# Kernel tuning notes

Hardware: AMD Instinct MI355X
Metric: run time of the kernel (lower is better)

The kernel has to match this reference:

```python
import jax, jax.numpy as jnp
import numpy as np

B, N, C = 2, 4096, 512
H = 8
K = 512  # num pivotal tokens


def setup_inputs() -> dict:
    key = jax.random.key(0)
    k1, k2, k3 = jax.random.split(key, 3)
    x = jax.random.normal(k1, (B, N, C), dtype=jnp.float32)
    w_qkv = jax.random.normal(k2, (C, 3 * C), dtype=jnp.float32) * (C ** -0.5)
    w_proj = jax.random.normal(k3, (C, C), dtype=jnp.float32) * (C ** -0.5)
    b_proj = jnp.zeros((C,), dtype=jnp.float32)
    return {"x": x, "w_qkv": w_qkv, "w_proj": w_proj, "b_proj": b_proj,
            "num_heads": H, "num_pivots": K}


def reference(x, w_qkv, w_proj, b_proj, num_heads, num_pivots):
    b, n, c = x.shape
    h = num_heads
    d = c // h
    scale = d ** -0.5
    # qkv projection -> q, k, v each [b, h, n, d]
    qkv = (x @ w_qkv).reshape(b, n, 3, h, d)
    q, k, v = jnp.moveaxis(qkv, 2, 0)          # each [b, n, h, d]
    q = jnp.swapaxes(q, 1, 2)                  # [b, h, n, d]
    k = jnp.swapaxes(k, 1, 2)
    v = jnp.swapaxes(v, 1, 2)
    # raw attention scores, materialized (the custom-kernel hotspot)
    attn = jax.nn.softmax(jnp.einsum('bhqd,bhkd->bhqk', q, k) * scale, axis=-1)
    # standard attention output + projection
    out = jnp.einsum('bhqk,bhkd->bhqd', attn, v)       # [b, h, n, d]
    out = jnp.swapaxes(out, 1, 2).reshape(b, n, c)     # [b, n, c]
    out = out @ w_proj + b_proj
    # pivotal-token importance: attention mass each token receives,
    # averaged over heads and queries -> [b, n]
    importance = attn.mean(axis=1).mean(axis=1)
    _, idx = jax.lax.top_k(importance, num_pivots)     # [b, K]
    # gather pivotal tokens -> reduced sequence [b, K, c]
    pivots = jnp.take_along_axis(out, idx[:, :, None], axis=1)
    return pivots
```

## Files before the change

kernel.cpp:

```cpp
#include <hip/hip_runtime.h>
#include <hip/hip_bf16.h>

#define BB 2
#define NN 4096
#define CC 512
#define HH 8
#define DD 64
#define KPIV 512
#define SCALE 0.125f
#define C2INV 4.8828125e-4f
#define C2    2048.0f

typedef unsigned short ushort_t;
typedef __attribute__((ext_vector_type(8))) short short8;
typedef __attribute__((ext_vector_type(8))) _Float16 half8;
typedef __attribute__((ext_vector_type(16))) float float16;

__device__ __forceinline__ float bf2f(ushort_t h) {
    union { unsigned u; float f; } x; x.u = ((unsigned)h) << 16; return x.f;
}
__device__ __forceinline__ ushort_t f2bf(float f) {
    __hip_bfloat16 h = __float2bfloat16(f);
    ushort_t u;
    __builtin_memcpy(&u, &h, sizeof(u));
    return u;
}
__device__ __forceinline__ void split2h(float x, _Float16& hi, _Float16& lo) {
    hi = (_Float16)x;
    lo = (_Float16)((x - (float)hi) * C2);
}

__global__ __launch_bounds__(256) void qkv_gemm_k(
    const float* __restrict__ x, const float* __restrict__ w,
    float* __restrict__ q, _Float16* __restrict__ khg, _Float16* __restrict__ klg,
    ushort_t* __restrict__ v)
{
    __shared__ __attribute__((aligned(16))) float xs[16][132];
    __shared__ __attribute__((aligned(16))) float ws[16][132];
    const int t = threadIdx.x;
    const int row0 = blockIdx.x * 128;
    const int col0 = blockIdx.y * 128;
    const int tr = t & 15, tc = t >> 4;
    const int ts = col0 >> 9;
    float acc[8][8] = {};
    for (int k0 = 0; k0 < CC; k0 += 16) {
        __syncthreads();
        {
            const int r = t >> 1, off = (t & 1) * 8;
            const float* xp = x + (size_t)(row0 + r) * CC + k0 + off;
            float4 v0 = *(const float4*)xp;
            float4 v1 = *(const float4*)(xp + 4);
            xs[off + 0][r] = v0.x; xs[off + 1][r] = v0.y;
            xs[off + 2][r] = v0.z; xs[off + 3][r] = v0.w;
            xs[off + 4][r] = v1.x; xs[off + 5][r] = v1.y;
            xs[off + 6][r] = v1.z; xs[off + 7][r] = v1.w;
        }
        {
            const int kk = t >> 4, c8 = (t & 15) * 8;
            const float* wp2 = w + (size_t)(k0 + kk) * (3 * CC) + col0 + c8;
            *(float4*)&ws[kk][c8]     = *(const float4*)wp2;
            *(float4*)&ws[kk][c8 + 4] = *(const float4*)(wp2 + 4);
        }
        __syncthreads();
        #pragma unroll
        for (int kk = 0; kk < 16; ++kk) {
            float a[8], b[8];
            *(float4*)&a[0] = *(const float4*)&xs[kk][tr * 8];
            *(float4*)&a[4] = *(const float4*)&xs[kk][tr * 8 + 4];
            *(float4*)&b[0] = *(const float4*)&ws[kk][tc * 8];
            *(float4*)&b[4] = *(const float4*)&ws[kk][tc * 8 + 4];
            #pragma unroll
            for (int i = 0; i < 8; ++i)
                #pragma unroll
                for (int j = 0; j < 8; ++j)
                    acc[i][j] = fmaf(a[i], b[j], acc[i][j]);
        }
    }
    const int gc0 = col0 + tc * 8;
    const int hh = (gc0 >> 6) & 7;
    const int dd0 = gc0 & 63;
    #pragma unroll
    for (int i = 0; i < 8; ++i) {
        const int grow = row0 + tr * 8 + i;
        const int b = grow >> 12, n = grow & (NN - 1);
        const size_t base = (((size_t)b * HH + hh) * NN + n) * DD + dd0;
        if (ts == 0) {
            float4 v0, v1;
            v0.x = acc[i][0]; v0.y = acc[i][1]; v0.z = acc[i][2]; v0.w = acc[i][3];
            v1.x = acc[i][4]; v1.y = acc[i][5]; v1.z = acc[i][6]; v1.w = acc[i][7];
            *(float4*)(q + base) = v0;
            *(float4*)(q + base + 4) = v1;
        } else if (ts == 1) {
            half8 h8, l8;
            #pragma unroll
            for (int j = 0; j < 8; ++j) {
                _Float16 a2, b2; split2h(acc[i][j], a2, b2);
                h8[j] = a2; l8[j] = b2;
            }
            *(half8*)(khg + base) = h8;
            *(half8*)(klg + base) = l8;
        } else {
            #pragma unroll
            for (int j = 0; j < 8; ++j)
                v[(((size_t)b * HH + hh) * DD + dd0 + j) * NN + n] = f2bf(acc[i][j]);
        }
    }
}


__device__ __forceinline__ void load_q_frags_h(
    const float* __restrict__ q, size_t row, int g, half8* qh, half8* ql)
{
    const float* qp = q + row * DD + g * 8;
    #pragma unroll
    for (int kd = 0; kd < 4; ++kd) {
        float4 f0 = *(const float4*)(qp + kd * 16);
        float4 f1 = *(const float4*)(qp + kd * 16 + 4);
        float xv[8] = {f0.x, f0.y, f0.z, f0.w, f1.x, f1.y, f1.z, f1.w};
        #pragma unroll
        for (int j = 0; j < 8; ++j) {
            _Float16 a2, b2; split2h(xv[j] * SCALE, a2, b2);
            qh[kd][j] = a2; ql[kd][j] = b2;
        }
    }
}

__device__ __forceinline__ void stage_k128(
    const _Float16* __restrict__ khg, const _Float16* __restrict__ klg,
    int bh, int n0, int t, half8* khs, half8* kls)
{
    const _Float16* kb = khg + ((size_t)bh * NN + n0) * DD;
    const _Float16* lb = klg + ((size_t)bh * NN + n0) * DD;
    #pragma unroll
    for (int j = 0; j < 4; ++j) {
        const int s = t + j * 256;
        const int seg = s >> 7, tok = s & 127;
        const size_t off = (size_t)tok * DD + seg * 8;
        uint4 uh = *(const uint4*)(kb + off);
        uint4 ul = *(const uint4*)(lb + off);
        *(uint4*)&khs[seg * 128 + tok] = uh;
        *(uint4*)&kls[seg * 128 + tok] = ul;
    }
}

#define S_MFMA_STEP(t0)                                                       \
    float16 a0, a12;                                                          \
    _Pragma("unroll")                                                         \
    for (int i = 0; i < 16; ++i) { a0[i] = 0.f; a12[i] = 0.f; }               \
    _Pragma("unroll")                                                         \
    for (int kd = 0; kd < 4; ++kd) {                                          \
        half8 bhi = khs[(kd * 2 + g) * 128 + (t0) + ln];                      \
        half8 blo = kls[(kd * 2 + g) * 128 + (t0) + ln];                      \
        a0  = __builtin_amdgcn_mfma_f32_32x32x16_f16(qh[kd], bhi, a0, 0,0,0); \
        a12 = __builtin_amdgcn_mfma_f32_32x32x16_f16(ql[kd], bhi, a12,0,0,0); \
        a12 = __builtin_amdgcn_mfma_f32_32x32x16_f16(qh[kd], blo, a12,0,0,0); \
    }

__global__ __launch_bounds__(256) void pass_a_k(
    const float* __restrict__ q, const _Float16* __restrict__ khg,
    const _Float16* __restrict__ klg, float* __restrict__ l)
{
    __shared__ half8 khs[8 * 128];
    __shared__ half8 kls[8 * 128];
    const int t = threadIdx.x;
    const int lane = t & 63, wv = t >> 6;
    const int g = lane >> 5, ln = lane & 31;
    const int bh = blockIdx.x >> 5;
    const int qt = blockIdx.x & 31;
    half8 qh[4], ql[4];
    load_q_frags_h(q, (size_t)bh * NN + qt * 128 + wv * 32 + ln, g, qh, ql);
    float rowacc[16];
    #pragma unroll
    for (int r = 0; r < 16; ++r) rowacc[r] = 0.f;
    for (int n0 = 0; n0 < NN; n0 += 128) {
        __syncthreads();
        stage_k128(khg, klg, bh, n0, t, khs, kls);
        __syncthreads();
        #pragma unroll
        for (int ii = 0; ii < 4; ++ii) {
            S_MFMA_STEP(ii * 32)
            #pragma unroll
            for (int r = 0; r < 16; ++r)
                rowacc[r] += __expf(fmaf(a12[r], C2INV, a0[r]));
        }
    }
    #pragma unroll
    for (int r = 0; r < 16; ++r) {
        float vs = rowacc[r];
        vs += __shfl_xor(vs, 1);
        vs += __shfl_xor(vs, 2);
        vs += __shfl_xor(vs, 4);
        vs += __shfl_xor(vs, 8);
        vs += __shfl_xor(vs, 16);
        rowacc[r] = vs;
    }
    if (ln == 0) {
        #pragma unroll
        for (int r = 0; r < 16; ++r) {
            const int row = (r & 3) + 8 * (r >> 2) + 4 * g;
            l[(size_t)bh * NN + qt * 128 + wv * 32 + row] = rowacc[r];
        }
    }
}

__global__ __launch_bounds__(256) void pass_b_k(
    const float* __restrict__ q, const _Float16* __restrict__ khg,
    const _Float16* __restrict__ klg, const float* __restrict__ l,
    float* __restrict__ colsum)
{
    __shared__ half8 khs[8 * 128];
    __shared__ half8 kls[8 * 128];
    __shared__ float colbuf[4][128];
    const int t = threadIdx.x;
    const int lane = t & 63, wv = t >> 6;
    const int g = lane >> 5, ln = lane & 31;
    const int bh = blockIdx.x >> 5;
    const int qt = blockIdx.x & 31;
    half8 qh[4], ql[4];
    load_q_frags_h(q, (size_t)bh * NN + qt * 128 + wv * 32 + ln, g, qh, ql);
    float rv[16];
    #pragma unroll
    for (int r = 0; r < 16; ++r) {
        const int row = (r & 3) + 8 * (r >> 2) + 4 * g;
        rv[r] = 1.0f / l[(size_t)bh * NN + qt * 128 + wv * 32 + row];
    }
    for (int n0 = 0; n0 < NN; n0 += 128) {
        __syncthreads();
        if (n0 > 0 && t < 128)
            colsum[(size_t)blockIdx.x * NN + (n0 - 128) + t] =
                (colbuf[0][t] + colbuf[1][t]) + (colbuf[2][t] + colbuf[3][t]);
        stage_k128(khg, klg, bh, n0, t, khs, kls);
        __syncthreads();
        #pragma unroll
        for (int ii = 0; ii < 4; ++ii) {
            S_MFMA_STEP(ii * 32)
            float cs = 0.f;
            #pragma unroll
            for (int r = 0; r < 16; ++r)
                cs = fmaf(__expf(fmaf(a12[r], C2INV, a0[r])), rv[r], cs);
            cs += __shfl_xor(cs, 32);
            if (g == 0) colbuf[wv][ii * 32 + ln] = cs;
        }
    }
    __syncthreads();
    if (t < 128)
        colsum[(size_t)blockIdx.x * NN + (NN - 128) + t] =
            (colbuf[0][t] + colbuf[1][t]) + (colbuf[2][t] + colbuf[3][t]);
}

__global__ __launch_bounds__(256) void imp_reduce_k(
    const float* __restrict__ colsum, double* __restrict__ imp)
{
    const int n = blockIdx.x * 256 + threadIdx.x;
    const int b = n >> 12, c = n & (NN - 1);
    const float* p = colsum + (size_t)b * 256 * NN + c;
    double s = 0.0;
    for (int i = 0; i < 256; ++i) s += (double)p[(size_t)i * NN];
    imp[n] = s * (1.0 / (double)(HH * NN));
}

__global__ __launch_bounds__(1024) void topk_k(
    const double* __restrict__ imp, int* __restrict__ idxout)
{
    __shared__ double sv[4096];
    __shared__ int si[4096];
    const int b = blockIdx.x, t = threadIdx.x;
    for (int i = t; i < 4096; i += 1024) { sv[i] = imp[b * 4096 + i]; si[i] = i; }
    __syncthreads();
    for (int kk = 2; kk <= 4096; kk <<= 1) {
        for (int j = kk >> 1; j > 0; j >>= 1) {
            #pragma unroll 1
            for (int r = 0; r < 2; ++r) {
                const int cm = t + r * 1024;
                const int i = ((cm & ~(j - 1)) << 1) | (cm & (j - 1));
                const int lo = i | j;
                const bool up = ((i & kk) == 0);
                const double va = sv[i], vb = sv[lo];
                const int ia = si[i], ib = si[lo];
                const bool after = (va < vb) || (va == vb && ia > ib);
                if (after == up) { sv[i] = vb; sv[lo] = va; si[i] = ib; si[lo] = ia; }
            }
            __syncthreads();
        }
    }
    if (t < KPIV) idxout[b * KPIV + t] = si[t];
}

__global__ __launch_bounds__(256) void pass_c_k(
    const float* __restrict__ q, const _Float16* __restrict__ khg,
    const _Float16* __restrict__ klg, const ushort_t* __restrict__ vt,
    const float* __restrict__ l, const int* __restrict__ idx,
    float* __restrict__ opiv)
{
    __shared__ short8 pfr[4][4][32];
    __shared__ __attribute__((aligned(16))) float osum[4][32][64];
    const int t = threadIdx.x;
    const int lane = t & 63, wv = t >> 6;
    const int g = lane >> 5, ln = lane & 31;
    const int bid = blockIdx.x;
    const int b = bid >> 8, h = (bid >> 5) & 7;
    const int chunk = (bid >> 1) & 15, th = bid & 1;
    const int bh = b * HH + h;
    const int r0 = chunk * 32;
    const int tokq = idx[b * KPIV + r0 + ln];
    half8 qh[4], ql[4];
    load_q_frags_h(q, (size_t)bh * NN + tokq, g, qh, ql);
    float rv[16];
    #pragma unroll
    for (int r = 0; r < 16; ++r) {
        const int row = (r & 3) + 8 * (r >> 2) + 4 * g;
        rv[r] = 1.0f / l[(size_t)bh * NN + idx[b * KPIV + r0 + row]];
    }
    float16 oacc0, oacc1;
    #pragma unroll
    for (int i = 0; i < 16; ++i) { oacc0[i] = 0.f; oacc1[i] = 0.f; }
    const int base_n = th * 2048 + wv * 512;
    for (int step = 0; step < 16; ++step) {
        const int n0 = base_n + step * 32;
        float16 a0, a12;
        #pragma unroll
        for (int i = 0; i < 16; ++i) { a0[i] = 0.f; a12[i] = 0.f; }
        const size_t koff = ((size_t)bh * NN + n0 + ln) * DD + g * 8;
        #pragma unroll
        for (int kd = 0; kd < 4; ++kd) {
            uint4 uh = *(const uint4*)(khg + koff + kd * 16);
            uint4 ul = *(const uint4*)(klg + koff + kd * 16);
            half8 bh8, bl8;
            __builtin_memcpy(&bh8, &uh, 16);
            __builtin_memcpy(&bl8, &ul, 16);
            a0  = __builtin_amdgcn_mfma_f32_32x32x16_f16(qh[kd], bh8, a0, 0,0,0);
            a12 = __builtin_amdgcn_mfma_f32_32x32x16_f16(ql[kd], bh8, a12,0,0,0);
            a12 = __builtin_amdgcn_mfma_f32_32x32x16_f16(qh[kd], bl8, a12,0,0,0);
        }
        __syncthreads();
        #pragma unroll
        for (int r = 0; r < 16; ++r) {
            const int row = (r & 3) + 8 * (r >> 2) + 4 * g;
            const float p = __expf(fmaf(a12[r], C2INV, a0[r])) * rv[r];
            *((ushort_t*)&pfr[wv][ln >> 3][row] + (ln & 7)) = f2bf(p);
        }
        __syncthreads();
        #pragma unroll
        for (int kh2 = 0; kh2 < 2; ++kh2) {
            short8 pa = pfr[wv][kh2 * 2 + g][ln];
            const ushort_t* vp0 = vt + ((size_t)bh * DD + ln) * NN + n0 + kh2 * 16 + g * 8;
            uint4 u0 = *(const uint4*)vp0;
            uint4 u1 = *(const uint4*)(vp0 + (size_t)32 * NN);
            short8 vb0, vb1;
            __builtin_memcpy(&vb0, &u0, 16);
            __builtin_memcpy(&vb1, &u1, 16);
            oacc0 = __builtin_amdgcn_mfma_f32_32x32x16_bf16(pa, vb0, oacc0, 0,0,0);
            oacc1 = __builtin_amdgcn_mfma_f32_32x32x16_bf16(pa, vb1, oacc1, 0,0,0);
        }
    }
    #pragma unroll
    for (int r = 0; r < 16; ++r) {
        const int row = (r & 3) + 8 * (r >> 2) + 4 * g;
        osum[wv][row][ln]      = oacc0[r];
        osum[wv][row][32 + ln] = oacc1[r];
    }
    __syncthreads();
    {
        const int qrow = t >> 3, d0 = (t & 7) * 8;
        float s[8] = {};
        #pragma unroll
        for (int w = 0; w < 4; ++w) {
            float4 a  = *(const float4*)&osum[w][qrow][d0];
            float4 b2 = *(const float4*)&osum[w][qrow][d0 + 4];
            s[0] += a.x;  s[1] += a.y;  s[2] += a.z;  s[3] += a.w;
            s[4] += b2.x; s[5] += b2.y; s[6] += b2.z; s[7] += b2.w;
        }
        float* op = opiv + ((size_t)(b * KPIV + r0 + qrow)) * CC + h * DD + d0;
        #pragma unroll
        for (int j = 0; j < 8; ++j) atomicAdd(op + j, s[j]);
    }
}

__global__ __launch_bounds__(256) void proj_k(
    const float* __restrict__ opiv, const float* __restrict__ wp,
    const float* __restrict__ bp, float* __restrict__ out)
{
    __shared__ __attribute__((aligned(16))) float os[8][CC];
    const int t = threadIdx.x;
    const int r0 = blockIdx.x * 8;
    for (int f = t; f < 1024; f += 256) {
        const int rr = f >> 7, i = (f & 127) * 4;
        *(float4*)&os[rr][i] = *(const float4*)(opiv + (size_t)(r0 + rr) * CC + i);
    }
    __syncthreads();
    const int c0 = t;
    float acc0[8] = {}, acc1[8] = {};
    for (int i = 0; i < CC; ++i) {
        const float w0 = wp[(size_t)i * CC + c0];
        const float w1 = wp[(size_t)i * CC + c0 + 256];
        #pragma unroll
        for (int rr = 0; rr < 8; ++rr) {
            const float ov = os[rr][i];
            acc0[rr] = fmaf(ov, w0, acc0[rr]);
            acc1[rr] = fmaf(ov, w1, acc1[rr]);
        }
    }
    const float b0 = bp[c0], b1 = bp[c0 + 256];
    #pragma unroll
    for (int rr = 0; rr < 8; ++rr) {
        out[((size_t)(r0 + rr)) * CC + c0]       = acc0[rr] + b0;
        out[((size_t)(r0 + rr)) * CC + c0 + 256] = acc1[rr] + b1;
    }
}

extern "C" void kernel_launch(void* const* d_in, const int* in_sizes, int n_in,
                              void* d_out, int out_size, void* d_ws, size_t ws_size,
                              hipStream_t stream)
{
    const float* x     = (const float*)d_in[0];
    const float* wqkv  = (const float*)d_in[1];
    const float* wproj = (const float*)d_in[2];
    const float* bproj = (const float*)d_in[3];

    float*     q      = (float*)d_ws;
    _Float16*  khg    = (_Float16*)(q + (size_t)BB * HH * NN * DD);
    _Float16*  klg    = khg + (size_t)BB * HH * NN * DD;
    ushort_t*  v      = (ushort_t*)(klg + (size_t)BB * HH * NN * DD);
    float*     l      = (float*)(v + (size_t)BB * HH * NN * DD);
    float*     colsum = l + (size_t)BB * HH * NN;
    double*    imp    = (double*)(colsum + (size_t)512 * NN);
    int*       idx    = (int*)(imp + BB * NN);
    float*     opiv   = (float*)(idx + BB * KPIV);
    float*     out    = (float*)d_out;

    const size_t need = (size_t)((char*)(opiv + (size_t)BB * KPIV * CC) - (char*)d_ws);
    if (ws_size < need) return;

    qkv_gemm_k<<<dim3(64, 12), 256, 0, stream>>>(x, wqkv, q, khg, klg, v);
    pass_a_k<<<512, 256, 0, stream>>>(q, khg, klg, l);
    pass_b_k<<<512, 256, 0, stream>>>(q, khg, klg, l, colsum);
    imp_reduce_k<<<32, 256, 0, stream>>>(colsum, imp);
    topk_k<<<2, 1024, 0, stream>>>(imp, idx);
    hipMemsetAsync(opiv, 0, (size_t)BB * KPIV * CC * sizeof(float), stream);
    pass_c_k<<<512, 256, 0, stream>>>(q, khg, klg, v, l, idx, opiv);
    proj_k<<<128, 256, 0, stream>>>(opiv, wproj, bproj, out);
}
```

Before: 689.4 us.

## Presplit Q into fp16 hi/lo in GEMM and read K directly from global

```diff
diff --git a/kernel.cpp b/kernel.cpp
--- a/kernel.cpp
+++ b/kernel.cpp
@@ -32,8 +32,9 @@
 
 __global__ __launch_bounds__(256) void qkv_gemm_k(
     const float* __restrict__ x, const float* __restrict__ w,
-    float* __restrict__ q, _Float16* __restrict__ khg, _Float16* __restrict__ klg,
-    ushort_t* __restrict__ v)
+    _Float16* __restrict__ qhg, _Float16* __restrict__ qlg,
+    _Float16* __restrict__ khg, _Float16* __restrict__ klg,
+    ushort_t* __restrict__ vt)
 {
     __shared__ __attribute__((aligned(16))) float xs[16][132];
     __shared__ __attribute__((aligned(16))) float ws[16][132];
@@ -85,11 +86,14 @@
         const int b = grow >> 12, n = grow & (NN - 1);
         const size_t base = (((size_t)b * HH + hh) * NN + n) * DD + dd0;
         if (ts == 0) {
-            float4 v0, v1;
-            v0.x = acc[i][0]; v0.y = acc[i][1]; v0.z = acc[i][2]; v0.w = acc[i][3];
-            v1.x = acc[i][4]; v1.y = acc[i][5]; v1.z = acc[i][6]; v1.w = acc[i][7];
-            *(float4*)(q + base) = v0;
-            *(float4*)(q + base + 4) = v1;
+            half8 h8, l8;
+            #pragma unroll
+            for (int j = 0; j < 8; ++j) {
+                _Float16 a2, b2; split2h(acc[i][j] * SCALE, a2, b2);
+                h8[j] = a2; l8[j] = b2;
+            }
+            *(half8*)(qhg + base) = h8;
+            *(half8*)(qlg + base) = l8;
         } else if (ts == 1) {
             half8 h8, l8;
             #pragma unroll
@@ -102,87 +106,58 @@
         } else {
             #pragma unroll
             for (int j = 0; j < 8; ++j)
-                v[(((size_t)b * HH + hh) * DD + dd0 + j) * NN + n] = f2bf(acc[i][j]);
-        }
-    }
-}
-
-
-__device__ __forceinline__ void load_q_frags_h(
-    const float* __restrict__ q, size_t row, int g, half8* qh, half8* ql)
-{
-    const float* qp = q + row * DD + g * 8;
+                vt[(((size_t)b * HH + hh) * DD + dd0 + j) * NN + n] = f2bf(acc[i][j]);
+        }
+    }
+}
+
+__device__ __forceinline__ void load_q_frags(
+    const _Float16* __restrict__ qhg, const _Float16* __restrict__ qlg,
+    size_t qrow, int g, half8* qh, half8* ql)
+{
+    const size_t off = qrow * DD + g * 8;
     #pragma unroll
     for (int kd = 0; kd < 4; ++kd) {
-        float4 f0 = *(const float4*)(qp + kd * 16);
-        float4 f1 = *(const float4*)(qp + kd * 16 + 4);
-        float xv[8] = {f0.x, f0.y, f0.z, f0.w, f1.x, f1.y, f1.z, f1.w};
-        #pragma unroll
-        for (int j = 0; j < 8; ++j) {
-            _Float16 a2, b2; split2h(xv[j] * SCALE, a2, b2);
-            qh[kd][j] = a2; ql[kd][j] = b2;
-        }
-    }
-}
-
-__device__ __forceinline__ void stage_k128(
+        qh[kd] = *(const half8*)(qhg + off + kd * 16);
+        ql[kd] = *(const half8*)(qlg + off + kd * 16);
+    }
+}
+
+#define S_STEP(koff)                                                           \
+    float16 a0, a12;                                                           \
+    _Pragma("unroll")                                                          \
+    for (int i = 0; i < 16; ++i) { a0[i] = 0.f; a12[i] = 0.f; }                \
+    _Pragma("unroll")                                                          \
+    for (int kd = 0; kd < 4; ++kd) {                                           \
+        half8 bh8 = *(const half8*)(khg + (koff) + kd * 16);                   \
+        half8 bl8 = *(const half8*)(klg + (koff) + kd * 16);                   \
+        a0  = __builtin_amdgcn_mfma_f32_32x32x16_f16(qh[kd], bh8, a0, 0,0,0);  \
+        a12 = __builtin_amdgcn_mfma_f32_32x32x16_f16(ql[kd], bh8, a12,0,0,0);  \
+        a12 = __builtin_amdgcn_mfma_f32_32x32x16_f16(qh[kd], bl8, a12,0,0,0);  \
+    }
+
+__global__ __launch_bounds__(256) void pass_a_k(
+    const _Float16* __restrict__ qhg, const _Float16* __restrict__ qlg,
     const _Float16* __restrict__ khg, const _Float16* __restrict__ klg,
-    int bh, int n0, int t, half8* khs, half8* kls)
-{
-    const _Float16* kb = khg + ((size_t)bh * NN + n0) * DD;
-    const _Float16* lb = klg + ((size_t)bh * NN + n0) * DD;
-    #pragma unroll
-    for (int j = 0; j < 4; ++j) {
-        const int s = t + j * 256;
-        const int seg = s >> 7, tok = s & 127;
-        const size_t off = (size_t)tok * DD + seg * 8;
-        uint4 uh = *(const uint4*)(kb + off);
-        uint4 ul = *(const uint4*)(lb + off);
-        *(uint4*)&khs[seg * 128 + tok] = uh;
-        *(uint4*)&kls[seg * 128 + tok] = ul;
-    }
-}
-
-#define S_MFMA_STEP(t0)                                                       \
-    float16 a0, a12;                                                          \
-    _Pragma("unroll")                                                         \
-    for (int i = 0; i < 16; ++i) { a0[i] = 0.f; a12[i] = 0.f; }               \
-    _Pragma("unroll")                                                         \
-    for (int kd = 0; kd < 4; ++kd) {                                          \
-        half8 bhi = khs[(kd * 2 + g) * 128 + (t0) + ln];                      \
-        half8 blo = kls[(kd * 2 + g) * 128 + (t0) + ln];                      \
-        a0  = __builtin_amdgcn_mfma_f32_32x32x16_f16(qh[kd], bhi, a0, 0,0,0); \
-        a12 = __builtin_amdgcn_mfma_f32_32x32x16_f16(ql[kd], bhi, a12,0,0,0); \
-        a12 = __builtin_amdgcn_mfma_f32_32x32x16_f16(qh[kd], blo, a12,0,0,0); \
-    }
-
-__global__ __launch_bounds__(256) void pass_a_k(
-    const float* __restrict__ q, const _Float16* __restrict__ khg,
-    const _Float16* __restrict__ klg, float* __restrict__ l)
-{
-    __shared__ half8 khs[8 * 128];
-    __shared__ half8 kls[8 * 128];
+    float* __restrict__ l)
+{
     const int t = threadIdx.x;
     const int lane = t & 63, wv = t >> 6;
     const int g = lane >> 5, ln = lane & 31;
     const int bh = blockIdx.x >> 5;
     const int qt = blockIdx.x & 31;
     half8 qh[4], ql[4];
-    load_q_frags_h(q, (size_t)bh * NN + qt * 128 + wv * 32 + ln, g, qh, ql);
+    load_q_frags(qhg, qlg, (size_t)bh * NN + qt * 128 + wv * 32 + ln, g, qh, ql);
     float rowacc[16];
     #pragma unroll
     for (int r = 0; r < 16; ++r) rowacc[r] = 0.f;
-    for (int n0 = 0; n0 < NN; n0 += 128) {
-        __syncthreads();
-        stage_k128(khg, klg, bh, n0, t, khs, kls);
-        __syncthreads();
-        #pragma unroll
-        for (int ii = 0; ii < 4; ++ii) {
-            S_MFMA_STEP(ii * 32)
-            #pragma unroll
-            for (int r = 0; r < 16; ++r)
-                rowacc[r] += __expf(fmaf(a12[r], C2INV, a0[r]));
-        }
+    #pragma unroll 2
+    for (int n0 = 0; n0 < NN; n0 += 32) {
+        const size_t koff = ((size_t)bh * NN + n0 + ln) * DD + g * 8;
+        S_STEP(koff)
+        #pragma unroll
+        for (int r = 0; r < 16; ++r)
+            rowacc[r] += __expf(fmaf(a12[r], C2INV, a0[r]));
     }
     #pragma unroll
     for (int r = 0; r < 16; ++r) {
@@ -204,48 +179,39 @@
 }
 
 __global__ __launch_bounds__(256) void pass_b_k(
-    const float* __restrict__ q, const _Float16* __restrict__ khg,
-    const _Float16* __restrict__ klg, const float* __restrict__ l,
-    float* __restrict__ colsum)
-{
-    __shared__ half8 khs[8 * 128];
-    __shared__ half8 kls[8 * 128];
-    __shared__ float colbuf[4][128];
+    const _Float16* __restrict__ qhg, const _Float16* __restrict__ qlg,
+    const _Float16* __restrict__ khg, const _Float16* __restrict__ klg,
+    const float* __restrict__ l, float* __restrict__ colsum)
+{
+    __shared__ float colbuf[4][NN];
     const int t = threadIdx.x;
     const int lane = t & 63, wv = t >> 6;
     const int g = lane >> 5, ln = lane & 31;
     const int bh = blockIdx.x >> 5;
     const int qt = blockIdx.x & 31;
     half8 qh[4], ql[4];
-    load_q_frags_h(q, (size_t)bh * NN + qt * 128 + wv * 32 + ln, g, qh, ql);
+    load_q_frags(qhg, qlg, (size_t)bh * NN + qt * 128 + wv * 32 + ln, g, qh, ql);
     float rv[16];
     #pragma unroll
     for (int r = 0; r < 16; ++r) {
         const int row = (r & 3) + 8 * (r >> 2) + 4 * g;
         rv[r] = 1.0f / l[(size_t)bh * NN + qt * 128 + wv * 32 + row];
     }
-    for (int n0 = 0; n0 < NN; n0 += 128) {
-        __syncthreads();
-        if (n0 > 0 && t < 128)
-            colsum[(size_t)blockIdx.x * NN + (n0 - 128) + t] =
-                (colbuf[0][t] + colbuf[1][t]) + (colbuf[2][t] + colbuf[3][t]);
-        stage_k128(khg, klg, bh, n0, t, khs, kls);
-        __syncthreads();
-        #pragma unroll
-        for (int ii = 0; ii < 4; ++ii) {
-            S_MFMA_STEP(ii * 32)
-            float cs = 0.f;
-            #pragma unroll
-            for (int r = 0; r < 16; ++r)
-                cs = fmaf(__expf(fmaf(a12[r], C2INV, a0[r])), rv[r], cs);
-            cs += __shfl_xor(cs, 32);
-            if (g == 0) colbuf[wv][ii * 32 + ln] = cs;
-        }
+    #pragma unroll 2
+    for (int n0 = 0; n0 < NN; n0 += 32) {
+        const size_t koff = ((size_t)bh * NN + n0 + ln) * DD + g * 8;
+        S_STEP(koff)
+        float cs = 0.f;
+        #pragma unroll
+        for (int r = 0; r < 16; ++r)
+            cs = fmaf(__expf(fmaf(a12[r], C2INV, a0[r])), rv[r], cs);
+        cs += __shfl_xor(cs, 32);
+        if (g == 0) colbuf[wv][n0 + ln] = cs;
     }
     __syncthreads();
-    if (t < 128)
-        colsum[(size_t)blockIdx.x * NN + (NN - 128) + t] =
-            (colbuf[0][t] + colbuf[1][t]) + (colbuf[2][t] + colbuf[3][t]);
+    for (int c = t; c < NN; c += 256)
+        colsum[(size_t)blockIdx.x * NN + c] =
+            (colbuf[0][c] + colbuf[1][c]) + (colbuf[2][c] + colbuf[3][c]);
 }
 
 __global__ __launch_bounds__(256) void imp_reduce_k(
@@ -287,10 +253,10 @@
 }
 
 __global__ __launch_bounds__(256) void pass_c_k(
-    const float* __restrict__ q, const _Float16* __restrict__ khg,
-    const _Float16* __restrict__ klg, const ushort_t* __restrict__ vt,
-    const float* __restrict__ l, const int* __restrict__ idx,
-    float* __restrict__ opiv)
+    const _Float16* __restrict__ qhg, const _Float16* __restrict__ qlg,
+    const _Float16* __restrict__ khg, const _Float16* __restrict__ klg,
+    const ushort_t* __restrict__ vt, const float* __restrict__ l,
+    const int* __restrict__ idx, float* __restrict__ opiv)
 {
     __shared__ short8 pfr[4][4][32];
     __shared__ __attribute__((aligned(16))) float osum[4][32][64];
@@ -304,7 +270,7 @@
     const int r0 = chunk * 32;
     const int tokq = idx[b * KPIV + r0 + ln];
     half8 qh[4], ql[4];
-    load_q_frags_h(q, (size_t)bh * NN + tokq, g, qh, ql);
+    load_q_frags(qhg, qlg, (size_t)bh * NN + tokq, g, qh, ql);
     float rv[16];
     #pragma unroll
     for (int r = 0; r < 16; ++r) {
@@ -317,21 +283,8 @@
     const int base_n = th * 2048 + wv * 512;
     for (int step = 0; step < 16; ++step) {
         const int n0 = base_n + step * 32;
-        float16 a0, a12;
-        #pragma unroll
-        for (int i = 0; i < 16; ++i) { a0[i] = 0.f; a12[i] = 0.f; }
         const size_t koff = ((size_t)bh * NN + n0 + ln) * DD + g * 8;
-        #pragma unroll
-        for (int kd = 0; kd < 4; ++kd) {
-            uint4 uh = *(const uint4*)(khg + koff + kd * 16);
-            uint4 ul = *(const uint4*)(klg + koff + kd * 16);
-            half8 bh8, bl8;
-            __builtin_memcpy(&bh8, &uh, 16);
-            __builtin_memcpy(&bl8, &ul, 16);
-            a0  = __builtin_amdgcn_mfma_f32_32x32x16_f16(qh[kd], bh8, a0, 0,0,0);
-            a12 = __builtin_amdgcn_mfma_f32_32x32x16_f16(ql[kd], bh8, a12,0,0,0);
-            a12 = __builtin_amdgcn_mfma_f32_32x32x16_f16(qh[kd], bl8, a12,0,0,0);
-        }
+        S_STEP(koff)
         __syncthreads();
         #pragma unroll
         for (int r = 0; r < 16; ++r) {
@@ -417,11 +370,13 @@
     const float* wproj = (const float*)d_in[2];
     const float* bproj = (const float*)d_in[3];
 
-    float*     q      = (float*)d_ws;
-    _Float16*  khg    = (_Float16*)(q + (size_t)BB * HH * NN * DD);
-    _Float16*  klg    = khg + (size_t)BB * HH * NN * DD;
-    ushort_t*  v      = (ushort_t*)(klg + (size_t)BB * HH * NN * DD);
-    float*     l      = (float*)(v + (size_t)BB * HH * NN * DD);
+    const size_t NE = (size_t)BB * HH * NN * DD;
+    _Float16*  qhg    = (_Float16*)d_ws;
+    _Float16*  qlg    = qhg + NE;
+    _Float16*  khg    = qlg + NE;
+    _Float16*  klg    = khg + NE;
+    ushort_t*  v      = (ushort_t*)(klg + NE);
+    float*     l      = (float*)(v + NE);
     float*     colsum = l + (size_t)BB * HH * NN;
     double*    imp    = (double*)(colsum + (size_t)512 * NN);
     int*       idx    = (int*)(imp + BB * NN);
@@ -431,12 +386,12 @@
     const size_t need = (size_t)((char*)(opiv + (size_t)BB * KPIV * CC) - (char*)d_ws);
     if (ws_size < need) return;
 
-    qkv_gemm_k<<<dim3(64, 12), 256, 0, stream>>>(x, wqkv, q, khg, klg, v);
-    pass_a_k<<<512, 256, 0, stream>>>(q, khg, klg, l);
-    pass_b_k<<<512, 256, 0, stream>>>(q, khg, klg, l, colsum);
+    qkv_gemm_k<<<dim3(64, 12), 256, 0, stream>>>(x, wqkv, qhg, qlg, khg, klg, v);
+    pass_a_k<<<512, 256, 0, stream>>>(qhg, qlg, khg, klg, l);
+    pass_b_k<<<512, 256, 0, stream>>>(qhg, qlg, khg, klg, l, colsum);
     imp_reduce_k<<<32, 256, 0, stream>>>(colsum, imp);
     topk_k<<<2, 1024, 0, stream>>>(imp, idx);
     hipMemsetAsync(opiv, 0, (size_t)BB * KPIV * CC * sizeof(float), stream);
-    pass_c_k<<<512, 256, 0, stream>>>(q, khg, klg, v, l, idx, opiv);
+    pass_c_k<<<512, 256, 0, stream>>>(qhg, qlg, khg, klg, v, l, idx, opiv);
     proj_k<<<128, 256, 0, stream>>>(opiv, wproj, bproj, out);
 }
```

New measurement: 863.2 us. +25.2%, slower.
